# Performance work log

Measured on AMD Instinct MI355X. Metric: run time of the kernel, lower is better.

The kernel has to match this reference:

```python
import jax, jax.numpy as jnp
import numpy as np

H = 16
DH = 64
THETA = 10000.0


def setup_inputs() -> dict:
    key = jax.random.key(0)
    ks = jax.random.split(key, 9)
    B, M, R = 4, 1024, 256
    d = H * DH
    s = 0.05
    return {
        "Pq": jax.random.normal(ks[0], (B, M, R), jnp.float32) * s,
        "Pk": jax.random.normal(ks[1], (B, M, R), jnp.float32) * s,
        "Pv": jax.random.normal(ks[2], (B, M, R), jnp.float32) * s,
        "Vq": jax.random.normal(ks[3], (R, d), jnp.float32) * s,
        "Vk": jax.random.normal(ks[4], (R, d), jnp.float32) * s,
        "Vv": jax.random.normal(ks[5], (R, d), jnp.float32) * s,
        "bq": jax.random.normal(ks[6], (d,), jnp.float32) * s,
        "bk": jax.random.normal(ks[7], (d,), jnp.float32) * s,
        "bv": jax.random.normal(ks[8], (d,), jnp.float32) * s,
        "attention_mask": jnp.ones((B, M), jnp.int32),
        "position_ids": jnp.tile(jnp.arange(M, dtype=jnp.int32), (B, 1)),
    }


def _rope_cos_sin(position_ids):
    # half-dim frequencies, matching the kernel's half-half rotation
    half = DH // 2
    inv_freq = 1.0 / (THETA ** (jnp.arange(0, half, dtype=jnp.float32) / half))
    ang = position_ids.astype(jnp.float32)[..., None] * inv_freq  # [B,M,half]
    return jnp.cos(ang), jnp.sin(ang)


def _rotate(x, cos, sin):
    # x: [B,H,M,dh]; cos/sin: [B,M,half] -> broadcast over heads
    half = DH // 2
    x0, x1 = x[..., :half], x[..., half:]
    c = cos[:, None, :, :]
    s = sin[:, None, :, :]
    return jnp.concatenate([x0 * c - x1 * s, x0 * s + x1 * c], axis=-1)


def reference(Pq, Pk, Pv, Vq, Vk, Vv, bq, bk, bv, attention_mask, position_ids):
    B, M, R = Pq.shape
    # reconstruct per-head Q/K/V from low-rank factors
    Vq3 = Vq.reshape(R, H, DH)
    Vk3 = Vk.reshape(R, H, DH)
    Vv3 = Vv.reshape(R, H, DH)
    q = jnp.einsum("bmr,rhd->bhmd", Pq, Vq3) + bq.reshape(H, DH)[None, :, None, :]
    k = jnp.einsum("bmr,rhd->bhmd", Pk, Vk3) + bk.reshape(H, DH)[None, :, None, :]
    v = jnp.einsum("bmr,rhd->bhmd", Pv, Vv3) + bv.reshape(H, DH)[None, :, None, :]
    cos, sin = _rope_cos_sin(position_ids)
    q = _rotate(q, cos, sin)
    k = _rotate(k, cos, sin)
    scale = 1.0 / jnp.sqrt(jnp.float32(DH))
    scores = jnp.einsum("bhmd,bhnd->bhmn", q, k) * scale  # [B,H,M,M]
    valid = attention_mask.astype(bool)
    pad = valid[:, None, :, None] & valid[:, None, None, :]
    scores = jnp.where(pad, scores, -jnp.inf)
    p = jax.nn.softmax(scores, axis=-1)
    out = jnp.einsum("bhmn,bhnd->bhmd", p, v)
    return out
```

## Files before the change

### kernel.cpp

```cpp
#include <hip/hip_runtime.h>
#include <hip/hip_bf16.h>
#include <math.h>

#define BB 4
#define MM 1024
#define RR 256
#define HH 16
#define DHH 64
#define DD (HH*DHH)

typedef __attribute__((ext_vector_type(8))) short short8;
typedef __attribute__((ext_vector_type(4))) float f32x4;

static __device__ __forceinline__ unsigned short f2bf(float x) {
    __hip_bfloat16 h = __float2bfloat16(x);
    return *(unsigned short*)&h;
}

#if defined(__has_builtin)
#  if __has_builtin(__builtin_amdgcn_exp2f)
#    define EXP2F(x) __builtin_amdgcn_exp2f(x)
#  endif
#endif
#ifndef EXP2F
#  define EXP2F(x) __expf((x) * 0.6931471805599453f)
#endif

static __device__ __forceinline__ unsigned pack_bf16_rh(float a, float b) {
    unsigned ua = __builtin_bit_cast(unsigned, a) + 0x8000u;
    unsigned ub = __builtin_bit_cast(unsigned, b) + 0x8000u;
    return __builtin_amdgcn_perm(ub, ua, 0x07060302u);
}

__global__ __launch_bounds__(256) void prep_kernel(
    const float* __restrict__ Pq, const float* __restrict__ Pk, const float* __restrict__ Pv,
    const float* __restrict__ Vq, const float* __restrict__ Vk, const float* __restrict__ Vv,
    __hip_bfloat16* __restrict__ VTq, __hip_bfloat16* __restrict__ VTk,
    __hip_bfloat16* __restrict__ VTv, __hip_bfloat16* __restrict__ Pb)
{
    const int t = threadIdx.x;
    if (blockIdx.x < 768) {
        const int z   = blockIdx.x / 256;
        const int rem = blockIdx.x % 256;
        const int r0  = (rem & 7) * 32;
        const int d0  = (rem >> 3) * 32;
        const float* V = (z == 0) ? Vq : (z == 1) ? Vk : Vv;
        __hip_bfloat16* VT = (z == 0) ? VTq : (z == 1) ? VTk : VTv;

        __shared__ __hip_bfloat16 Ts[32][33];
        {
            const int row = t >> 3;
            const int c4  = (t & 7) * 4;
            float4 f = *(const float4*)&V[(size_t)(r0 + row) * DD + d0 + c4];
            Ts[row][c4 + 0] = __float2bfloat16(f.x);
            Ts[row][c4 + 1] = __float2bfloat16(f.y);
            Ts[row][c4 + 2] = __float2bfloat16(f.z);
            Ts[row][c4 + 3] = __float2bfloat16(f.w);
        }
        __syncthreads();
        {
            const int orow = t >> 3;
            const int oc4  = (t & 7) * 4;
            union { unsigned short u[4]; uint2 v; } pk;
            #pragma unroll
            for (int i = 0; i < 4; ++i) pk.u[i] = *(unsigned short*)&Ts[oc4 + i][orow];
            *(uint2*)&VT[(size_t)(d0 + orow) * RR + r0 + oc4] = pk.v;
        }
    } else {
        const size_t n4 = (size_t)BB * MM * RR / 4;
        size_t i = (size_t)(blockIdx.x - 768) * 256 + t;
        const int which = (int)(i / n4);
        const size_t off = i - (size_t)which * n4;
        const float* P = (which == 0) ? Pq : (which == 1) ? Pk : Pv;
        float4 f = *(const float4*)(P + off * 4);
        union { unsigned short u[4]; uint2 v; } pk;
        pk.u[0] = f2bf(f.x); pk.u[1] = f2bf(f.y); pk.u[2] = f2bf(f.z); pk.u[3] = f2bf(f.w);
        *(uint2*)((unsigned short*)Pb + (size_t)which * BB * MM * RR + off * 4) = pk.v;
    }
}

__global__ __launch_bounds__(256) void svd_gemm(
    const __hip_bfloat16* __restrict__ Pb,
    const __hip_bfloat16* __restrict__ VTq, const __hip_bfloat16* __restrict__ VTk,
    const __hip_bfloat16* __restrict__ VTv,
    const float* __restrict__ bq, const float* __restrict__ bk, const float* __restrict__ bv,
    const int* __restrict__ pos_ids,
    __hip_bfloat16* __restrict__ qout, __hip_bfloat16* __restrict__ kout,
    __hip_bfloat16* __restrict__ vTout)
{
    const int which = blockIdx.z;
    const short* P = (const short*)Pb + (size_t)which * BB * MM * RR;
    const __hip_bfloat16* VT = (which == 0) ? VTq : (which == 1) ? VTk : VTv;
    const float* bias        = (which == 0) ? bq : (which == 1) ? bk : bv;

    const int h   = blockIdx.y;
    const int bm0 = blockIdx.x * 256;
    const int b   = bm0 >> 10;
    const int m0  = bm0 & 1023;
    const int tid = threadIdx.x;
    const int lane = tid & 63;
    const int w    = tid >> 6;
    const int l15  = lane & 15;
    const int quad = lane >> 4;

    __shared__ alignas(16) short SM[256 * 72 + 64 * 72];
    short* As = SM;
    short* Bs = SM + 256 * 72;

    f32x4 acc[4][4];
    #pragma unroll
    for (int mt = 0; mt < 4; ++mt)
        #pragma unroll
        for (int dt = 0; dt < 4; ++dt) acc[mt][dt] = (f32x4){0.f, 0.f, 0.f, 0.f};

    for (int kc = 0; kc < 4; ++kc) {
        #pragma unroll
        for (int i = 0; i < 8; ++i) {
            int u = tid + i * 256;
            int row = u >> 3;
            int cg  = (u & 7) * 8;
            *(uint4*)&As[row * 72 + cg] =
                *(const uint4*)&P[(size_t)(bm0 + row) * RR + kc * 64 + cg];
        }
        #pragma unroll
        for (int i = 0; i < 2; ++i) {
            int u = tid + i * 256;
            int row = u >> 3;
            int cg  = (u & 7) * 8;
            *(uint4*)&Bs[row * 72 + cg] =
                *(const uint4*)((const short*)VT + (size_t)(h * 64 + row) * RR + kc * 64 + cg);
        }
        __syncthreads();

        #pragma unroll
        for (int ks = 0; ks < 2; ++ks) {
            short8 a[4];
            #pragma unroll
            for (int mt = 0; mt < 4; ++mt)
                a[mt] = *(const short8*)&As[(w * 64 + mt * 16 + l15) * 72 + ks * 32 + quad * 8];
            #pragma unroll
            for (int dt = 0; dt < 4; ++dt) {
                short8 bf = *(const short8*)&Bs[(dt * 16 + l15) * 72 + ks * 32 + quad * 8];
                #pragma unroll
                for (int mt = 0; mt < 4; ++mt)
                    acc[mt][dt] = __builtin_amdgcn_mfma_f32_16x16x32_bf16(a[mt], bf, acc[mt][dt], 0, 0, 0);
            }
        }
        __syncthreads();
    }

    #pragma unroll
    for (int dt = 0; dt < 4; ++dt) {
        float bc = bias[h * 64 + dt * 16 + l15];
        #pragma unroll
        for (int mt = 0; mt < 4; ++mt)
            #pragma unroll
            for (int r = 0; r < 4; ++r) acc[mt][dt][r] += bc;
    }

    if (which < 2) {
        __hip_bfloat16* out = (which == 0) ? qout : kout;
        int pm[4][4];
        #pragma unroll
        for (int mt = 0; mt < 4; ++mt)
            #pragma unroll
            for (int r = 0; r < 4; ++r)
                pm[mt][r] = pos_ids[bm0 + w * 64 + mt * 16 + quad * 4 + r];
        float cB[2][4][4], sB[2][4][4];
        #pragma unroll
        for (int f2 = 0; f2 < 2; ++f2) {
            float invf = __powf(10000.0f, -(float)(f2 * 16 + l15) * (1.0f / 32.0f));
            #pragma unroll
            for (int mt = 0; mt < 4; ++mt)
                #pragma unroll
                for (int r = 0; r < 4; ++r) {
                    float ang = (float)pm[mt][r] * invf;
                    __sincosf(ang, &sB[f2][mt][r], &cB[f2][mt][r]);
                }
        }
        #pragma unroll
        for (int dt = 0; dt < 4; ++dt) {
            const int cd = dt * 16 + l15;
            const int f2 = dt & 1;
            #pragma unroll
            for (int mt = 0; mt < 4; ++mt)
                #pragma unroll
                for (int r = 0; r < 4; ++r) {
                    float x  = acc[mt][dt][r];
                    float xp = acc[mt][dt ^ 2][r];
                    float c = cB[f2][mt][r], s = sB[f2][mt][r];
                    float val = (dt < 2) ? (x * c - xp * s) : (xp * s + x * c);
                    int m = m0 + w * 64 + mt * 16 + quad * 4 + r;
                    out[(((size_t)b * HH + h) * MM + m) * DHH + cd] = __float2bfloat16(val);
                }
        }
    } else {
        short* Tt = SM;
        __syncthreads();
        #pragma unroll
        for (int dt = 0; dt < 4; ++dt)
            #pragma unroll
            for (int mt = 0; mt < 4; ++mt) {
                union { unsigned short u[4]; uint2 v; } pk;
                #pragma unroll
                for (int r = 0; r < 4; ++r) pk.u[r] = f2bf(acc[mt][dt][r]);
                *(uint2*)&Tt[(dt * 16 + l15) * 264 + w * 64 + mt * 16 + quad * 4] = pk.v;
            }
        __syncthreads();
        #pragma unroll
        for (int it = 0; it < 8; ++it) {
            int u = tid + it * 256;
            int row = u >> 5;
            int seg = u & 31;
            *(uint4*)&vTout[(((size_t)b * HH + h) * DHH + row) * MM + m0 + seg * 8] =
                *(const uint4*)&Tt[row * 264 + seg * 8];
        }
    }
}

__global__ __launch_bounds__(256, 2) void attn_kernel(
    const __hip_bfloat16* __restrict__ q, const __hip_bfloat16* __restrict__ k,
    const __hip_bfloat16* __restrict__ vT,
    const int* __restrict__ mask, float* __restrict__ out)
{
    const int bh   = blockIdx.x & 63;
    const int qt   = blockIdx.x >> 6;
    const int b    = bh >> 4;
    const int tid  = threadIdx.x;
    const int lane = tid & 63;
    const int w    = tid >> 6;
    const int l15  = lane & 15;
    const int quad = lane >> 4;
    const int q0   = qt * 128;

    __shared__ alignas(16) __hip_bfloat16 Kt[128][72];
    __shared__ alignas(16) __hip_bfloat16 Vt[64][136];

    const short* kbase = (const short*)k  + (size_t)bh * MM * DHH;
    const short* vbase = (const short*)vT + (size_t)bh * DHH * MM;

    short8 qa[2][2];
    #pragma unroll
    for (int mt = 0; mt < 2; ++mt) {
        const short* qb = (const short*)q +
            ((size_t)bh * MM + q0 + w * 32 + mt * 16 + l15) * DHH + quad * 8;
        qa[mt][0] = *(const short8*)(qb);
        qa[mt][1] = *(const short8*)(qb + 32);
    }

    f32x4 Ot[2][4];
    #pragma unroll
    for (int mt = 0; mt < 2; ++mt)
        #pragma unroll
        for (int dt = 0; dt < 4; ++dt) Ot[mt][dt] = (f32x4){0.f, 0.f, 0.f, 0.f};
    float lsum[2] = {0.f, 0.f};

    const int* maskb = mask + b * MM;
    const int srcbase = (lane & 48) | ((lane & 48) >> 2);
    const float k2 = 0.125f * 1.44269504089f;

    for (int nc = 0; nc < MM / 128; ++nc) {
        const int n0 = nc * 128;
        #pragma unroll
        for (int pass = 0; pass < 4; ++pass) {
            int u   = tid + pass * 256;
            int row = u >> 3;
            int cg  = u & 7;
            *(uint4*)&Kt[row][cg * 8] =
                *(const uint4*)(kbase + (size_t)(n0 + row) * DHH + cg * 8);
        }
        #pragma unroll
        for (int pass = 0; pass < 4; ++pass) {
            int u   = tid + pass * 256;
            int row = u >> 4;
            int c   = u & 15;
            union { uint4 q4; uint2 h2[2]; } vld;
            vld.q4 = *(const uint4*)(vbase + (size_t)row * MM + n0 + c * 8);
            int g  = c >> 3;
            int c6 = c & 7;
            int base0 = g * 64 + (c6 >> 2) * 32 + (c6 & 1) * 16 + ((c6 >> 1) & 1) * 4;
            *(uint2*)&Vt[row][base0]     = vld.h2[0];
            *(uint2*)&Vt[row][base0 + 8] = vld.h2[1];
        }
        __syncthreads();

        unsigned long long bal0 = __ballot(maskb[n0 + lane] != 0);
        unsigned long long bal1 = __ballot(maskb[n0 + 64 + lane] != 0);

        f32x4 S[2][8];
        #pragma unroll
        for (int t = 0; t < 8; ++t) {
            const short* kr = (const short*)&Kt[t * 16 + l15][quad * 8];
            short8 ka0 = *(const short8*)(kr);
            short8 ka1 = *(const short8*)(kr + 32);
            #pragma unroll
            for (int mt = 0; mt < 2; ++mt) {
                f32x4 c = (f32x4){0.f, 0.f, 0.f, 0.f};
                c = __builtin_amdgcn_mfma_f32_16x16x32_bf16(ka0, qa[mt][0], c, 0, 0, 0);
                c = __builtin_amdgcn_mfma_f32_16x16x32_bf16(ka1, qa[mt][1], c, 0, 0, 0);
                S[mt][t] = c;
            }
        }

        #pragma unroll
        for (int t = 0; t < 8; ++t) {
            unsigned bits = (unsigned)((t < 4 ? bal0 : bal1) >> ((t & 3) * 16 + quad * 4));
            #pragma unroll
            for (int r = 0; r < 4; ++r) {
                float sb = ((bits >> r) & 1u) ? 0.0f : -1e30f;
                #pragma unroll
                for (int mt = 0; mt < 2; ++mt) {
                    float e = EXP2F(fmaf(S[mt][t][r], k2, sb));
                    lsum[mt] += e;
                    S[mt][t][r] = e;
                }
            }
        }

        short8 pa[2][4];
        #pragma unroll
        for (int mt = 0; mt < 2; ++mt)
            #pragma unroll
            for (int p = 0; p < 4; ++p) {
                union { unsigned u[4]; short8 s; } pk;
                pk.u[0] = pack_bf16_rh(S[mt][2*p][0],   S[mt][2*p][1]);
                pk.u[1] = pack_bf16_rh(S[mt][2*p][2],   S[mt][2*p][3]);
                pk.u[2] = pack_bf16_rh(S[mt][2*p+1][0], S[mt][2*p+1][1]);
                pk.u[3] = pack_bf16_rh(S[mt][2*p+1][2], S[mt][2*p+1][3]);
                pa[mt][p] = pk.s;
            }

        #pragma unroll
        for (int p = 0; p < 4; ++p) {
            #pragma unroll
            for (int dt = 0; dt < 4; ++dt) {
                short8 vb = *(const short8*)&Vt[dt * 16 + l15][p * 32 + quad * 8];
                #pragma unroll
                for (int mt = 0; mt < 2; ++mt)
                    Ot[mt][dt] = __builtin_amdgcn_mfma_f32_16x16x32_bf16(pa[mt][p], vb, Ot[mt][dt], 0, 0, 0);
            }
        }
        __syncthreads();
    }

    #pragma unroll
    for (int mt = 0; mt < 2; ++mt) {
        float s = lsum[mt];
        s += __shfl_xor(s, 16, 64);
        s += __shfl_xor(s, 32, 64);
        float inv = 1.0f / s;
        float* ob = out + ((size_t)bh * MM + q0 + w * 32 + mt * 16) * DHH;
        #pragma unroll
        for (int r = 0; r < 4; ++r) {
            float ir = __shfl(inv, srcbase + r, 64);
            #pragma unroll
            for (int dt = 0; dt < 4; ++dt)
                ob[(quad * 4 + r) * DHH + dt * 16 + l15] = Ot[mt][dt][r] * ir;
        }
    }
}

extern "C" void kernel_launch(void* const* d_in, const int* in_sizes, int n_in,
                              void* d_out, int out_size, void* d_ws, size_t ws_size,
                              hipStream_t stream) {
    const float* Pq = (const float*)d_in[0];
    const float* Pk = (const float*)d_in[1];
    const float* Pv = (const float*)d_in[2];
    const float* Vq = (const float*)d_in[3];
    const float* Vk = (const float*)d_in[4];
    const float* Vv = (const float*)d_in[5];
    const float* bq = (const float*)d_in[6];
    const float* bk = (const float*)d_in[7];
    const float* bv = (const float*)d_in[8];
    const int* mask = (const int*)d_in[9];
    const int* pos  = (const int*)d_in[10];
    float* out = (float*)d_out;

    const size_t qkv_elems = (size_t)BB * HH * MM * DHH;
    __hip_bfloat16* qb  = (__hip_bfloat16*)d_ws;
    __hip_bfloat16* kb  = qb + qkv_elems;
    __hip_bfloat16* vT  = kb + qkv_elems;
    __hip_bfloat16* VTq = vT + qkv_elems;
    __hip_bfloat16* VTk = VTq + (size_t)DD * RR;
    __hip_bfloat16* VTv = VTk + (size_t)DD * RR;
    __hip_bfloat16* Pb  = VTv + (size_t)DD * RR;

    prep_kernel<<<768 + 3 * BB * MM * RR / 4 / 256, 256, 0, stream>>>(
        Pq, Pk, Pv, Vq, Vk, Vv, VTq, VTk, VTv, Pb);

    dim3 gG(BB * MM / 256, HH, 3);
    svd_gemm<<<gG, 256, 0, stream>>>(Pb, VTq, VTk, VTv, bq, bk, bv, pos, qb, kb, vT);

    attn_kernel<<<BB * HH * (MM / 128), 256, 0, stream>>>(qb, kb, vT, mask, out);
}
```

Baseline: 133.9 us.

## Fuse P fp32-to-bf16 conversion into GEMM and double-buffer attention K/V tiles

Drops the separate conversion of Pq/Pk/Pv to bf16 in the prep kernel. The projection GEMM now loads fp32 P and converts it while staging into shared memory, which removes a global write and re-read of the bf16 copy. The attention kernel now double-buffers its K and V tiles in LDS: the next chunk is loaded into registers early and written to the alternate buffer after compute. This overlaps global loads with MFMA work, at the cost of doubling LDS use and adding register pressure, which may lower occupancy.

```diff
diff --git a/kernel.cpp b/kernel.cpp
--- a/kernel.cpp
+++ b/kernel.cpp
@@ -33,54 +33,41 @@
 }
 
 __global__ __launch_bounds__(256) void prep_kernel(
-    const float* __restrict__ Pq, const float* __restrict__ Pk, const float* __restrict__ Pv,
     const float* __restrict__ Vq, const float* __restrict__ Vk, const float* __restrict__ Vv,
     __hip_bfloat16* __restrict__ VTq, __hip_bfloat16* __restrict__ VTk,
-    __hip_bfloat16* __restrict__ VTv, __hip_bfloat16* __restrict__ Pb)
+    __hip_bfloat16* __restrict__ VTv)
 {
     const int t = threadIdx.x;
-    if (blockIdx.x < 768) {
-        const int z   = blockIdx.x / 256;
-        const int rem = blockIdx.x % 256;
-        const int r0  = (rem & 7) * 32;
-        const int d0  = (rem >> 3) * 32;
-        const float* V = (z == 0) ? Vq : (z == 1) ? Vk : Vv;
-        __hip_bfloat16* VT = (z == 0) ? VTq : (z == 1) ? VTk : VTv;
-
-        __shared__ __hip_bfloat16 Ts[32][33];
-        {
-            const int row = t >> 3;
-            const int c4  = (t & 7) * 4;
-            float4 f = *(const float4*)&V[(size_t)(r0 + row) * DD + d0 + c4];
-            Ts[row][c4 + 0] = __float2bfloat16(f.x);
-            Ts[row][c4 + 1] = __float2bfloat16(f.y);
-            Ts[row][c4 + 2] = __float2bfloat16(f.z);
-            Ts[row][c4 + 3] = __float2bfloat16(f.w);
-        }
-        __syncthreads();
-        {
-            const int orow = t >> 3;
-            const int oc4  = (t & 7) * 4;
-            union { unsigned short u[4]; uint2 v; } pk;
-            #pragma unroll
-            for (int i = 0; i < 4; ++i) pk.u[i] = *(unsigned short*)&Ts[oc4 + i][orow];
-            *(uint2*)&VT[(size_t)(d0 + orow) * RR + r0 + oc4] = pk.v;
-        }
-    } else {
-        const size_t n4 = (size_t)BB * MM * RR / 4;
-        size_t i = (size_t)(blockIdx.x - 768) * 256 + t;
-        const int which = (int)(i / n4);
-        const size_t off = i - (size_t)which * n4;
-        const float* P = (which == 0) ? Pq : (which == 1) ? Pk : Pv;
-        float4 f = *(const float4*)(P + off * 4);
+    const int z   = blockIdx.x / 256;
+    const int rem = blockIdx.x % 256;
+    const int r0  = (rem & 7) * 32;
+    const int d0  = (rem >> 3) * 32;
+    const float* V = (z == 0) ? Vq : (z == 1) ? Vk : Vv;
+    __hip_bfloat16* VT = (z == 0) ? VTq : (z == 1) ? VTk : VTv;
+
+    __shared__ __hip_bfloat16 Ts[32][33];
+    {
+        const int row = t >> 3;
+        const int c4  = (t & 7) * 4;
+        float4 f = *(const float4*)&V[(size_t)(r0 + row) * DD + d0 + c4];
+        Ts[row][c4 + 0] = __float2bfloat16(f.x);
+        Ts[row][c4 + 1] = __float2bfloat16(f.y);
+        Ts[row][c4 + 2] = __float2bfloat16(f.z);
+        Ts[row][c4 + 3] = __float2bfloat16(f.w);
+    }
+    __syncthreads();
+    {
+        const int orow = t >> 3;
+        const int oc4  = (t & 7) * 4;
         union { unsigned short u[4]; uint2 v; } pk;
-        pk.u[0] = f2bf(f.x); pk.u[1] = f2bf(f.y); pk.u[2] = f2bf(f.z); pk.u[3] = f2bf(f.w);
-        *(uint2*)((unsigned short*)Pb + (size_t)which * BB * MM * RR + off * 4) = pk.v;
+        #pragma unroll
+        for (int i = 0; i < 4; ++i) pk.u[i] = *(unsigned short*)&Ts[oc4 + i][orow];
+        *(uint2*)&VT[(size_t)(d0 + orow) * RR + r0 + oc4] = pk.v;
     }
 }
 
 __global__ __launch_bounds__(256) void svd_gemm(
-    const __hip_bfloat16* __restrict__ Pb,
+    const float* __restrict__ Pq, const float* __restrict__ Pk, const float* __restrict__ Pv,
     const __hip_bfloat16* __restrict__ VTq, const __hip_bfloat16* __restrict__ VTk,
     const __hip_bfloat16* __restrict__ VTv,
     const float* __restrict__ bq, const float* __restrict__ bk, const float* __restrict__ bv,
@@ -89,7 +76,7 @@
     __hip_bfloat16* __restrict__ vTout)
 {
     const int which = blockIdx.z;
-    const short* P = (const short*)Pb + (size_t)which * BB * MM * RR;
+    const float* P = (which == 0) ? Pq : (which == 1) ? Pk : Pv;
     const __hip_bfloat16* VT = (which == 0) ? VTq : (which == 1) ? VTk : VTv;
     const float* bias        = (which == 0) ? bq : (which == 1) ? bk : bv;
 
@@ -119,8 +106,15 @@
             int u = tid + i * 256;
             int row = u >> 3;
             int cg  = (u & 7) * 8;
-            *(uint4*)&As[row * 72 + cg] =
-                *(const uint4*)&P[(size_t)(bm0 + row) * RR + kc * 64 + cg];
+            const float* ps = P + (size_t)(bm0 + row) * RR + kc * 64 + cg;
+            float4 f0 = *(const float4*)ps;
+            float4 f1 = *(const float4*)(ps + 4);
+            union { unsigned short us[8]; uint4 v; } pk;
+            pk.us[0] = f2bf(f0.x); pk.us[1] = f2bf(f0.y);
+            pk.us[2] = f2bf(f0.z); pk.us[3] = f2bf(f0.w);
+            pk.us[4] = f2bf(f1.x); pk.us[5] = f2bf(f1.y);
+            pk.us[6] = f2bf(f1.z); pk.us[7] = f2bf(f1.w);
+            *(uint4*)&As[row * 72 + cg] = pk.v;
         }
         #pragma unroll
         for (int i = 0; i < 2; ++i) {
@@ -233,8 +227,8 @@
     const int quad = lane >> 4;
     const int q0   = qt * 128;
 
-    __shared__ alignas(16) __hip_bfloat16 Kt[128][72];
-    __shared__ alignas(16) __hip_bfloat16 Vt[64][136];
+    __shared__ alignas(16) __hip_bfloat16 Kt[2][128][72];
+    __shared__ alignas(16) __hip_bfloat16 Vt[2][64][136];
 
     const short* kbase = (const short*)k  + (size_t)bh * MM * DHH;
     const short* vbase = (const short*)vT + (size_t)bh * DHH * MM;
@@ -259,38 +253,53 @@
     const int srcbase = (lane & 48) | ((lane & 48) >> 2);
     const float k2 = 0.125f * 1.44269504089f;
 
+    {
+        #pragma unroll
+        for (int pass = 0; pass < 4; ++pass) {
+            int u = tid + pass * 256, row = u >> 3, cg = u & 7;
+            *(uint4*)&Kt[0][row][cg * 8] =
+                *(const uint4*)(kbase + (size_t)row * DHH + cg * 8);
+        }
+        #pragma unroll
+        for (int pass = 0; pass < 4; ++pass) {
+            int u = tid + pass * 256, row = u >> 4, c = u & 15;
+            union { uint4 q4; uint2 h2[2]; } vld;
+            vld.q4 = *(const uint4*)(vbase + (size_t)row * MM + c * 8);
+            int g = c >> 3, c6 = c & 7;
+            int base0 = g * 64 + (c6 >> 2) * 32 + (c6 & 1) * 16 + ((c6 >> 1) & 1) * 4;
+            *(uint2*)&Vt[0][row][base0]     = vld.h2[0];
+            *(uint2*)&Vt[0][row][base0 + 8] = vld.h2[1];
+        }
+        __syncthreads();
+    }
+
+    #pragma unroll 2
     for (int nc = 0; nc < MM / 128; ++nc) {
-        const int n0 = nc * 128;
-        #pragma unroll
-        for (int pass = 0; pass < 4; ++pass) {
-            int u   = tid + pass * 256;
-            int row = u >> 3;
-            int cg  = u & 7;
-            *(uint4*)&Kt[row][cg * 8] =
-                *(const uint4*)(kbase + (size_t)(n0 + row) * DHH + cg * 8);
-        }
-        #pragma unroll
-        for (int pass = 0; pass < 4; ++pass) {
-            int u   = tid + pass * 256;
-            int row = u >> 4;
-            int c   = u & 15;
-            union { uint4 q4; uint2 h2[2]; } vld;
-            vld.q4 = *(const uint4*)(vbase + (size_t)row * MM + n0 + c * 8);
-            int g  = c >> 3;
-            int c6 = c & 7;
-            int base0 = g * 64 + (c6 >> 2) * 32 + (c6 & 1) * 16 + ((c6 >> 1) & 1) * 4;
-            *(uint2*)&Vt[row][base0]     = vld.h2[0];
-            *(uint2*)&Vt[row][base0 + 8] = vld.h2[1];
-        }
-        __syncthreads();
-
-        unsigned long long bal0 = __ballot(maskb[n0 + lane] != 0);
-        unsigned long long bal1 = __ballot(maskb[n0 + 64 + lane] != 0);
+        const int cur = nc & 1;
+        const int n0  = nc * 128;
+
+        uint4 kreg[4], vreg[4];
+        if (nc < 7) {
+            const short* kb2 = kbase + (size_t)(n0 + 128) * DHH;
+            #pragma unroll
+            for (int pass = 0; pass < 4; ++pass) {
+                int u = tid + pass * 256, row = u >> 3, cg = u & 7;
+                kreg[pass] = *(const uint4*)(kb2 + (size_t)row * DHH + cg * 8);
+            }
+            const short* vb2 = vbase + n0 + 128;
+            #pragma unroll
+            for (int pass = 0; pass < 4; ++pass) {
+                int u = tid + pass * 256, row = u >> 4, c = u & 15;
+                vreg[pass] = *(const uint4*)(vb2 + (size_t)row * MM + c * 8);
+            }
+        }
+        int mv0 = maskb[n0 + lane];
+        int mv1 = maskb[n0 + 64 + lane];
 
         f32x4 S[2][8];
         #pragma unroll
         for (int t = 0; t < 8; ++t) {
-            const short* kr = (const short*)&Kt[t * 16 + l15][quad * 8];
+            const short* kr = (const short*)&Kt[cur][t * 16 + l15][quad * 8];
             short8 ka0 = *(const short8*)(kr);
             short8 ka1 = *(const short8*)(kr + 32);
             #pragma unroll
@@ -301,6 +310,17 @@
                 S[mt][t] = c;
             }
         }
+
+        if (nc < 7) {
+            #pragma unroll
+            for (int pass = 0; pass < 4; ++pass) {
+                int u = tid + pass * 256, row = u >> 3, cg = u & 7;
+                *(uint4*)&Kt[cur ^ 1][row][cg * 8] = kreg[pass];
+            }
+        }
+
+        unsigned long long bal0 = __ballot(mv0 != 0);
+        unsigned long long bal1 = __ballot(mv1 != 0);
 
         #pragma unroll
         for (int t = 0; t < 8; ++t) {
@@ -334,10 +354,23 @@
         for (int p = 0; p < 4; ++p) {
             #pragma unroll
             for (int dt = 0; dt < 4; ++dt) {
-                short8 vb = *(const short8*)&Vt[dt * 16 + l15][p * 32 + quad * 8];
+                short8 vb = *(const short8*)&Vt[cur][dt * 16 + l15][p * 32 + quad * 8];
                 #pragma unroll
                 for (int mt = 0; mt < 2; ++mt)
                     Ot[mt][dt] = __builtin_amdgcn_mfma_f32_16x16x32_bf16(pa[mt][p], vb, Ot[mt][dt], 0, 0, 0);
+            }
+        }
+
+        if (nc < 7) {
+            #pragma unroll
+            for (int pass = 0; pass < 4; ++pass) {
+                int u = tid + pass * 256, row = u >> 4, c = u & 15;
+                union { uint4 q4; uint2 h2[2]; } vld;
+                vld.q4 = vreg[pass];
+                int g = c >> 3, c6 = c & 7;
+                int base0 = g * 64 + (c6 >> 2) * 32 + (c6 & 1) * 16 + ((c6 >> 1) & 1) * 4;
+                *(uint2*)&Vt[cur ^ 1][row][base0]     = vld.h2[0];
+                *(uint2*)&Vt[cur ^ 1][row][base0 + 8] = vld.h2[1];
             }
         }
         __syncthreads();
@@ -383,13 +416,11 @@
     __hip_bfloat16* VTq = vT + qkv_elems;
     __hip_bfloat16* VTk = VTq + (size_t)DD * RR;
     __hip_bfloat16* VTv = VTk + (size_t)DD * RR;
-    __hip_bfloat16* Pb  = VTv + (size_t)DD * RR;
-
-    prep_kernel<<<768 + 3 * BB * MM * RR / 4 / 256, 256, 0, stream>>>(
-        Pq, Pk, Pv, Vq, Vk, Vv, VTq, VTk, VTv, Pb);
+
+    prep_kernel<<<768, 256, 0, stream>>>(Vq, Vk, Vv, VTq, VTk, VTv);
 
     dim3 gG(BB * MM / 256, HH, 3);
-    svd_gemm<<<gG, 256, 0, stream>>>(Pb, VTq, VTk, VTv, bq, bk, bv, pos, qb, kb, vT);
+    svd_gemm<<<gG, 256, 0, stream>>>(Pq, Pk, Pv, VTq, VTk, VTv, bq, bk, bv, pos, qb, kb, vT);
 
     attn_kernel<<<BB * HH * (MM / 128), 256, 0, stream>>>(qb, kb, vT, mask, out);
 }
```

New measurement: 145.7 us. +8.8%, slower.

## Double-buffer K/V tiles with direct global-to-LDS loads and XOR swizzle

Applied to the files above, without the earlier changes.

The attention loop now double-buffers the K and V tiles in LDS. The next K tile is prefetched with global_load_lds directly into an XOR-swizzled layout, and the next V tile is loaded into registers and stored after the PV MFMAs. This aims to hide global load latency behind compute, drop one barrier per iteration, and avoid bank conflicts without padding. s_setprio is raised around the MFMA blocks. LDS use roughly doubles, which may hurt the two-blocks-per-CU occupancy, and the held V registers raise register pressure.

```diff
diff --git a/kernel.cpp b/kernel.cpp
--- a/kernel.cpp
+++ b/kernel.cpp
@@ -30,6 +30,12 @@
     unsigned ua = __builtin_bit_cast(unsigned, a) + 0x8000u;
     unsigned ub = __builtin_bit_cast(unsigned, b) + 0x8000u;
     return __builtin_amdgcn_perm(ub, ua, 0x07060302u);
+}
+
+static __device__ __forceinline__ void gload_lds16(const void* g, void* l) {
+    __builtin_amdgcn_global_load_lds(
+        (const __attribute__((address_space(1))) unsigned int*)g,
+        (__attribute__((address_space(3))) unsigned int*)l, 16, 0, 0);
 }
 
 __global__ __launch_bounds__(256) void prep_kernel(
@@ -233,8 +239,8 @@
     const int quad = lane >> 4;
     const int q0   = qt * 128;
 
-    __shared__ alignas(16) __hip_bfloat16 Kt[128][72];
-    __shared__ alignas(16) __hip_bfloat16 Vt[64][136];
+    __shared__ alignas(16) short KtL[2][128 * 64];
+    __shared__ alignas(16) __hip_bfloat16 Vt[2][64][136];
 
     const short* kbase = (const short*)k  + (size_t)bh * MM * DHH;
     const short* vbase = (const short*)vT + (size_t)bh * DHH * MM;
@@ -259,40 +265,63 @@
     const int srcbase = (lane & 48) | ((lane & 48) >> 2);
     const float k2 = 0.125f * 1.44269504089f;
 
+    const int p0 = quad ^ (l15 & 7);
+    const int p1 = (quad + 4) ^ (l15 & 7);
+
+    {
+        #pragma unroll
+        for (int pass = 0; pass < 4; ++pass) {
+            int u = tid + pass * 256;
+            int row = u >> 3;
+            int gl  = (u & 7) ^ (row & 7);
+            gload_lds16(kbase + (size_t)row * DHH + gl * 8, &KtL[0][u * 8]);
+        }
+        #pragma unroll
+        for (int pass = 0; pass < 4; ++pass) {
+            int u = tid + pass * 256;
+            int row = u >> 4, c = u & 15;
+            union { uint4 q4; uint2 h2[2]; } vld;
+            vld.q4 = *(const uint4*)(vbase + (size_t)row * MM + c * 8);
+            int g = c >> 3, c6 = c & 7;
+            int base0 = g * 64 + (c6 >> 2) * 32 + (c6 & 1) * 16 + ((c6 >> 1) & 1) * 4;
+            *(uint2*)&Vt[0][row][base0]     = vld.h2[0];
+            *(uint2*)&Vt[0][row][base0 + 8] = vld.h2[1];
+        }
+        __syncthreads();
+    }
+
     for (int nc = 0; nc < MM / 128; ++nc) {
-        const int n0 = nc * 128;
-        #pragma unroll
-        for (int pass = 0; pass < 4; ++pass) {
-            int u   = tid + pass * 256;
-            int row = u >> 3;
-            int cg  = u & 7;
-            *(uint4*)&Kt[row][cg * 8] =
-                *(const uint4*)(kbase + (size_t)(n0 + row) * DHH + cg * 8);
-        }
-        #pragma unroll
-        for (int pass = 0; pass < 4; ++pass) {
-            int u   = tid + pass * 256;
-            int row = u >> 4;
-            int c   = u & 15;
-            union { uint4 q4; uint2 h2[2]; } vld;
-            vld.q4 = *(const uint4*)(vbase + (size_t)row * MM + n0 + c * 8);
-            int g  = c >> 3;
-            int c6 = c & 7;
-            int base0 = g * 64 + (c6 >> 2) * 32 + (c6 & 1) * 16 + ((c6 >> 1) & 1) * 4;
-            *(uint2*)&Vt[row][base0]     = vld.h2[0];
-            *(uint2*)&Vt[row][base0 + 8] = vld.h2[1];
-        }
-        __syncthreads();
+        const int cur = nc & 1;
+        const int n0  = nc * 128;
+
+        uint4 vreg[4];
+        if (nc < 7) {
+            const short* vb2 = vbase + n0 + 128;
+            #pragma unroll
+            for (int pass = 0; pass < 4; ++pass) {
+                int u = tid + pass * 256, row = u >> 4, c = u & 15;
+                vreg[pass] = *(const uint4*)(vb2 + (size_t)row * MM + c * 8);
+            }
+            const short* kb2 = kbase + (size_t)(n0 + 128) * DHH;
+            #pragma unroll
+            for (int pass = 0; pass < 4; ++pass) {
+                int u = tid + pass * 256;
+                int row = u >> 3;
+                int gl  = (u & 7) ^ (row & 7);
+                gload_lds16(kb2 + (size_t)row * DHH + gl * 8, &KtL[cur ^ 1][u * 8]);
+            }
+        }
 
         unsigned long long bal0 = __ballot(maskb[n0 + lane] != 0);
         unsigned long long bal1 = __ballot(maskb[n0 + 64 + lane] != 0);
 
         f32x4 S[2][8];
+        __builtin_amdgcn_s_setprio(1);
         #pragma unroll
         for (int t = 0; t < 8; ++t) {
-            const short* kr = (const short*)&Kt[t * 16 + l15][quad * 8];
-            short8 ka0 = *(const short8*)(kr);
-            short8 ka1 = *(const short8*)(kr + 32);
+            const short* krow = &KtL[cur][(t * 16 + l15) * 64];
+            short8 ka0 = *(const short8*)(krow + p0 * 8);
+            short8 ka1 = *(const short8*)(krow + p1 * 8);
             #pragma unroll
             for (int mt = 0; mt < 2; ++mt) {
                 f32x4 c = (f32x4){0.f, 0.f, 0.f, 0.f};
@@ -301,6 +330,7 @@
                 S[mt][t] = c;
             }
         }
+        __builtin_amdgcn_s_setprio(0);
 
         #pragma unroll
         for (int t = 0; t < 8; ++t) {
@@ -330,14 +360,29 @@
                 pa[mt][p] = pk.s;
             }
 
+        __builtin_amdgcn_s_setprio(1);
         #pragma unroll
         for (int p = 0; p < 4; ++p) {
             #pragma unroll
             for (int dt = 0; dt < 4; ++dt) {
-                short8 vb = *(const short8*)&Vt[dt * 16 + l15][p * 32 + quad * 8];
+                short8 vb = *(const short8*)&Vt[cur][dt * 16 + l15][p * 32 + quad * 8];
                 #pragma unroll
                 for (int mt = 0; mt < 2; ++mt)
                     Ot[mt][dt] = __builtin_amdgcn_mfma_f32_16x16x32_bf16(pa[mt][p], vb, Ot[mt][dt], 0, 0, 0);
+            }
+        }
+        __builtin_amdgcn_s_setprio(0);
+
+        if (nc < 7) {
+            #pragma unroll
+            for (int pass = 0; pass < 4; ++pass) {
+                int u = tid + pass * 256, row = u >> 4, c = u & 15;
+                union { uint4 q4; uint2 h2[2]; } vld;
+                vld.q4 = vreg[pass];
+                int g = c >> 3, c6 = c & 7;
+                int base0 = g * 64 + (c6 >> 2) * 32 + (c6 & 1) * 16 + ((c6 >> 1) & 1) * 4;
+                *(uint2*)&Vt[cur ^ 1][row][base0]     = vld.h2[0];
+                *(uint2*)&Vt[cur ^ 1][row][base0 + 8] = vld.h2[1];
             }
         }
         __syncthreads();
```

Measured after the change: 131.5 us. About the same (-1.8%).
